# Optimization experiments

Measured on AMD Instinct MI355X. Metric: run time of the kernel, lower is better.

## Reference

```python
import jax, jax.numpy as jnp
import numpy as np

N = 50000      # nodes
E = 800000     # edges (avg degree 16)
NE = 100000    # query edges
IN = 128; HID = 128; OUT = 128; FEAT = 2


def _linear_params(k, fan_in, fan_out):
    # torch.nn.Linear default init: U(-1/sqrt(fan_in), 1/sqrt(fan_in))
    s = 1.0 / np.sqrt(fan_in)
    k1, k2 = jax.random.split(k)
    W = jax.random.uniform(k1, (fan_in, fan_out), jnp.float32, -s, s)
    b = jax.random.uniform(k2, (fan_out,), jnp.float32, -s, s)
    return W, b


def setup_inputs() -> dict:
    key = jax.random.key(0)
    ks = jax.random.split(key, 9)
    inp = {}
    inp["x"] = jax.random.normal(ks[0], (N, IN), jnp.float32)
    inp["adj_t"] = jax.random.randint(ks[1], (2, E), 0, N)          # edge_index [2,E]
    inp["train_edges"] = jax.random.randint(ks[2], (NE, 2), 0, N)   # query edges
    # GCNConv stack params (lin weight + bias per layer)
    inp["W1"], inp["b1"] = _linear_params(ks[3], IN, HID)
    inp["W2"], inp["b2"] = _linear_params(ks[4], HID, HID)
    inp["W3"], inp["b3"] = _linear_params(ks[5], HID, OUT)
    # LinkPredictor MLP params
    inp["P1"], inp["pb1"] = _linear_params(ks[6], OUT, HID)
    inp["P2"], inp["pb2"] = _linear_params(ks[7], HID, HID)
    inp["P3"], inp["pb3"] = _linear_params(ks[8], HID, FEAT)
    return inp


def gcn_conv(x, edge_index, W, b):
    # GCNConv(normalize=False), edge_weight=None:
    #   h = x @ W; out[dst] += h[src]; out += bias
    h = x @ W                                    # [N, d_out]
    msg = h[edge_index[0]]                       # gather  [E, d_out]
    out = jax.ops.segment_sum(msg, edge_index[1], num_segments=x.shape[0])
    return out + b


def reference(x, adj_t, train_edges, W1, b1, W2, b2, W3, b3, P1, pb1, P2, pb2, P3, pb3):
    # GCN trunk (eval mode -> dropout is identity; dropout=0 anyway)
    h = jax.nn.relu(gcn_conv(x, adj_t, W1, b1))
    h = jax.nn.relu(gcn_conv(h, adj_t, W2, b2))
    emb = gcn_conv(h, adj_t, W3, b3)             # [N, OUT]
    # LinkPredictor on (src, dst) node-embedding pairs
    z = emb[train_edges[:, 0]] * emb[train_edges[:, 1]]   # [NE, OUT]
    z = jax.nn.relu(z @ P1 + pb1)
    z = jax.nn.relu(z @ P2 + pb2)
    z = z @ P3 + pb3                                       # [NE, FEAT]
    # F.normalize(p=2, dim=-1) with eps=1e-12
    z = z / jnp.maximum(jnp.linalg.norm(z, axis=-1, keepdims=True), 1e-12)
    pred = jax.nn.log_softmax(z, axis=-1)
    return pred[None]                                      # torch.unsqueeze(pred, 0)
```

## Files before the change

kernel.cpp:

```cpp
#include <hip/hip_runtime.h>
#include <math.h>

#define N_NODES 50000
#define N_EDGES 800000
#define N_QE    100000
#define D       128
#define NB      391
#define PCHUNK  8192

typedef _Float16 half8 __attribute__((ext_vector_type(8)));
typedef short    short8 __attribute__((ext_vector_type(8)));
typedef float    f32x4 __attribute__((ext_vector_type(4)));

static __device__ inline short f2bf(float f) {
    unsigned u = __builtin_bit_cast(unsigned, f);
    u += 0x7FFFu + ((u >> 16) & 1u);
    return (short)(u >> 16);
}

static const size_t O_BCNT = 0;
static const size_t O_OFF  = 256u * 1024;
static const size_t O_BC   = 512u * 1024;
static const size_t O_BB   = 768u * 1024;
static const size_t O_SRC  = 1024u * 1024;
static const size_t O_TMP  = 4u << 20;
static const size_t O_G    = 8u << 20;
static const size_t O_H    = O_G + 12800000u;
static const size_t O_T    = O_H + 12800000u;


__global__ __launch_bounds__(256)
void k_bcount(const int* __restrict__ dst, int* __restrict__ bcnt) {
    __shared__ int h[NB];
    const int t = threadIdx.x;
    const int e0 = blockIdx.x * PCHUNK;
    const int e1 = (e0 + PCHUNK < N_EDGES) ? e0 + PCHUNK : N_EDGES;
    for (int b = t; b < NB; b += 256) h[b] = 0;
    __syncthreads();
    for (int e = e0 + t; e < e1; e += 256)
        atomicAdd(&h[dst[e] >> 7], 1);
    __syncthreads();
    for (int b = t; b < NB; b += 256)
        if (h[b]) atomicAdd(&bcnt[b], h[b]);
}

__global__ __launch_bounds__(512)
void k_bscan(const int* __restrict__ bcnt, int* __restrict__ bbase,
             int* __restrict__ bcur, int* __restrict__ off) {
    __shared__ int sh[512];
    const int t = threadIdx.x;
    int v = (t < NB) ? bcnt[t] : 0;
    sh[t] = v;
    __syncthreads();
    #pragma unroll
    for (int o = 1; o < 512; o <<= 1) {
        int u = (t >= o) ? sh[t - o] : 0;
        __syncthreads();
        sh[t] += u;
        __syncthreads();
    }
    if (t < NB) { int e = sh[t] - v; bbase[t] = e; bcur[t] = e; }
    if (t == 0) { bbase[NB] = N_EDGES; off[N_NODES] = N_EDGES; }
}

__global__ __launch_bounds__(256)
void k_part(const int* __restrict__ src, const int* __restrict__ dst,
            int* __restrict__ bcur, unsigned* __restrict__ tmp)
{
    __shared__ int hcnt[NB];
    __shared__ int lpos[NB];
    __shared__ int base[NB];
    const int t = threadIdx.x;
    const int e0 = blockIdx.x * PCHUNK;
    const int e1 = (e0 + PCHUNK < N_EDGES) ? e0 + PCHUNK : N_EDGES;

    for (int b = t; b < NB; b += 256) { hcnt[b] = 0; lpos[b] = 0; }
    __syncthreads();
    for (int e = e0 + t; e < e1; e += 256)
        atomicAdd(&hcnt[dst[e] >> 7], 1);
    __syncthreads();
    for (int b = t; b < NB; b += 256) {
        int c = hcnt[b];
        base[b] = c ? atomicAdd(&bcur[b], c) : 0;
    }
    __syncthreads();
    for (int e = e0 + t; e < e1; e += 256) {
        int d = dst[e];
        int b = d >> 7;
        int pos = atomicAdd(&lpos[b], 1);
        tmp[base[b] + pos] = (unsigned)src[e] | ((unsigned)(d & 127) << 16);
    }
}

__global__ __launch_bounds__(256)
void k_fine2(const unsigned* __restrict__ tmp, const int* __restrict__ bbase,
             unsigned short* __restrict__ srcs, int* __restrict__ off)
{
    __shared__ int ncnt[128];
    __shared__ int fcur[128];
    const int t = threadIdx.x;
    const int b = blockIdx.x;
    const int n0 = b << 7;
    const int nn = (N_NODES - n0 < 128) ? N_NODES - n0 : 128;
    const int r0 = bbase[b];
    const int r1 = bbase[b + 1];

    if (t < 128) ncnt[t] = 0;
    __syncthreads();
    for (int i = r0 + t; i < r1; i += 256)
        atomicAdd(&ncnt[tmp[i] >> 16], 1);
    __syncthreads();
    int c = (t < 128) ? ncnt[t] : 0;
    #pragma unroll
    for (int o = 1; o < 128; o <<= 1) {
        int u = (t >= o && t < 128) ? ncnt[t - o] : 0;
        __syncthreads();
        if (t < 128) ncnt[t] += u;
        __syncthreads();
    }
    if (t < 128) {
        int excl = r0 + ncnt[t] - c;
        fcur[t] = excl;
        if (t < nn) off[n0 + t] = excl;
    }
    __syncthreads();
    for (int i = r0 + t; i < r1; i += 256) {
        unsigned en = tmp[i];
        int p = atomicAdd(&fcur[en >> 16], 1);
        srcs[p] = (unsigned short)(en & 0xFFFFu);
    }
}

__global__ __launch_bounds__(256)
void k_t16all(const float* __restrict__ W1, const float* __restrict__ W2,
              const float* __restrict__ W3, const float* __restrict__ Q1,
              const float* __restrict__ Q2, short* __restrict__ T)
{
    int m = blockIdx.x >> 6;
    const float* S = (m == 0) ? W1 : (m == 1) ? W2 : (m == 2) ? W3
                   : (m == 3) ? Q1 : Q2;
    short* Dp = T + m * 16384;
    int idx = (blockIdx.x & 63) * 256 + threadIdx.x;
    int c = idx & 127, k = idx >> 7;
    Dp[c * 128 + k] = f2bf(S[k * 128 + c]);
}


template<typename XT>
__global__ __launch_bounds__(256)
void k_mm(const XT* __restrict__ X, const short* __restrict__ WT,
          _Float16* __restrict__ Y, int rows)
{
    __shared__ __align__(16) short xs[64 * 128];
    const int tid = threadIdx.x;
    const int l   = tid & 63;
    const int w   = tid >> 6;
    const int g   = l >> 4;
    const int l15 = l & 15;
    const int row0 = blockIdx.x * 64;

    {
        int r = tid >> 2;
        int gr = row0 + r; if (gr >= rows) gr = rows - 1;
        const XT* src = X + (size_t)gr * D;
        #pragma unroll
        for (int it = 0; it < 4; ++it) {
            int s = (tid & 3) + it * 4;
            short8 h;
            if constexpr (sizeof(XT) == 4) {
                float4 v0 = *(const float4*)((const float*)src + s * 8);
                float4 v1 = *(const float4*)((const float*)src + s * 8 + 4);
                h[0] = f2bf(v0.x); h[1] = f2bf(v0.y);
                h[2] = f2bf(v0.z); h[3] = f2bf(v0.w);
                h[4] = f2bf(v1.x); h[5] = f2bf(v1.y);
                h[6] = f2bf(v1.z); h[7] = f2bf(v1.w);
            } else {
                half8 v = *(const half8*)((const _Float16*)src + s * 8);
                #pragma unroll
                for (int c = 0; c < 8; ++c) h[c] = f2bf((float)v[c]);
            }
            *(short8*)&xs[r * 128 + ((s ^ (r & 7)) * 8)] = h;
        }
    }

    short8 wf[2][4];
    #pragma unroll
    for (int tt = 0; tt < 2; ++tt) {
        int c = w * 32 + tt * 16 + l15;
        #pragma unroll
        for (int s = 0; s < 4; ++s)
            wf[tt][s] = *(const short8*)(WT + (size_t)c * 128 + s * 32 + g * 8);
    }

    __syncthreads();

    f32x4 acc[4][2];
    #pragma unroll
    for (int rt = 0; rt < 4; ++rt)
        #pragma unroll
        for (int tt = 0; tt < 2; ++tt)
            acc[rt][tt] = (f32x4){0.f, 0.f, 0.f, 0.f};

    #pragma unroll
    for (int rt = 0; rt < 4; ++rt) {
        const int r = rt * 16 + l15;
        short8 a[4];
        #pragma unroll
        for (int s = 0; s < 4; ++s) {
            int slot = (4 * s + g) ^ (r & 7);
            a[s] = *(const short8*)&xs[r * 128 + slot * 8];
        }
        #pragma unroll
        for (int tt = 0; tt < 2; ++tt)
            #pragma unroll
            for (int s = 0; s < 4; ++s)
                acc[rt][tt] = __builtin_amdgcn_mfma_f32_16x16x32_bf16(
                    a[s], wf[tt][s], acc[rt][tt], 0, 0, 0);
    }

    __syncthreads();

    #pragma unroll
    for (int rt = 0; rt < 4; ++rt)
        #pragma unroll
        for (int tt = 0; tt < 2; ++tt) {
            int c = w * 32 + tt * 16 + l15;
            #pragma unroll
            for (int i = 0; i < 4; ++i) {
                int row = rt * 16 + g * 4 + i;
                int slot = (c >> 3) ^ (row & 7);
                xs[row * 128 + slot * 8 + (c & 7)] =
                    (short)__builtin_bit_cast(unsigned short, (_Float16)acc[rt][tt][i]);
            }
        }
    __syncthreads();

    {
        int r = tid >> 2;
        int gr = row0 + r;
        if (gr < rows) {
            short* dstp = (short*)(Y + (size_t)gr * D);
            #pragma unroll
            for (int it = 0; it < 4; ++it) {
                int s = (tid & 3) + it * 4;
                *(short8*)(dstp + s * 8) =
                    *(const short8*)&xs[r * 128 + ((s ^ (r & 7)) * 8)];
            }
        }
    }
}

template<bool RELU>
__global__ __launch_bounds__(256)
void k_agg(const _Float16* __restrict__ Hin, const int* __restrict__ off,
           const unsigned short* __restrict__ srcs, const float* __restrict__ bias,
           _Float16* __restrict__ Hout)
{
    const int lane = threadIdx.x & 63;
    const int es   = lane >> 4;
    const int q    = lane & 15;
    const int wv   = threadIdx.x >> 6;
    const int n    = blockIdx.x * 4 + wv;
    const int j0 = __builtin_amdgcn_readfirstlane(off[n]);
    const int j1 = __builtin_amdgcn_readfirstlane(off[n + 1]);

    float acc[8] = {};
    int j = j0;

    for (; j + 16 <= j1; j += 16) {
        half8 v[4];
        #pragma unroll
        for (int k = 0; k < 4; ++k) {
            int s = srcs[j + 4 * k + es];
            v[k] = *(const half8*)(Hin + (size_t)s * D + q * 8);
        }
        #pragma unroll
        for (int k = 0; k < 4; ++k)
            #pragma unroll
            for (int c = 0; c < 8; ++c) acc[c] += (float)v[k][c];
    }
    for (; j + 4 <= j1; j += 4) {
        int s = srcs[j + es];
        half8 v = *(const half8*)(Hin + (size_t)s * D + q * 8);
        #pragma unroll
        for (int c = 0; c < 8; ++c) acc[c] += (float)v[c];
    }
    {
        int rem = j1 - j;
        if (rem > 0) {
            int s = srcs[j + (es < rem ? es : rem - 1)];
            half8 v = *(const half8*)(Hin + (size_t)s * D + q * 8);
            if (es < rem) {
                #pragma unroll
                for (int c = 0; c < 8; ++c) acc[c] += (float)v[c];
            }
        }
    }

    #pragma unroll
    for (int c = 0; c < 8; ++c) {
        acc[c] += __shfl_xor(acc[c], 16, 64);
        acc[c] += __shfl_xor(acc[c], 32, 64);
    }

    if (es == 0) {
        half8 o;
        #pragma unroll
        for (int c = 0; c < 8; ++c) {
            float t = acc[c] + bias[q * 8 + c];
            if (RELU) t = fmaxf(t, 0.f);
            o[c] = (_Float16)t;
        }
        *(half8*)(Hout + (size_t)n * D + q * 8) = o;
    }
}

__global__ __launch_bounds__(256)
void k_predm(const _Float16* __restrict__ emb, const int* __restrict__ te,
             const short* __restrict__ P1T, const float* __restrict__ pb1,
             const short* __restrict__ P2T, const float* __restrict__ pb2,
             const float* __restrict__ P3, const float* __restrict__ pb3,
             float* __restrict__ out)
{
    __shared__ __align__(16) short xs[64 * 128];
    __shared__ float red[64][8];
    const int tid = threadIdx.x;
    const int l   = tid & 63;
    const int w   = tid >> 6;
    const int g   = l >> 4;
    const int l15 = l & 15;
    const int row0 = blockIdx.x * 64;

    {
        int r = tid >> 2;
        int e = row0 + r; if (e >= N_QE) e = N_QE - 1;
        const int2 ee = *(const int2*)(te + 2 * e);
        const _Float16* sp = emb + (size_t)ee.x * D;
        const _Float16* dp = emb + (size_t)ee.y * D;
        #pragma unroll
        for (int it = 0; it < 4; ++it) {
            int s = (tid & 3) + it * 4;
            half8 a = *(const half8*)(sp + s * 8);
            half8 b = *(const half8*)(dp + s * 8);
            short8 h;
            #pragma unroll
            for (int c = 0; c < 8; ++c) h[c] = f2bf((float)a[c] * (float)b[c]);
            *(short8*)&xs[r * 128 + ((s ^ (r & 7)) * 8)] = h;
        }
    }
    __syncthreads();

    f32x4 acc[4][2];

    {
        short8 wf[2][4];
        #pragma unroll
        for (int tt = 0; tt < 2; ++tt) {
            int c = w * 32 + tt * 16 + l15;
            #pragma unroll
            for (int s = 0; s < 4; ++s)
                wf[tt][s] = *(const short8*)(P1T + (size_t)c * 128 + s * 32 + g * 8);
        }
        #pragma unroll
        for (int rt = 0; rt < 4; ++rt)
            #pragma unroll
            for (int tt = 0; tt < 2; ++tt)
                acc[rt][tt] = (f32x4){0.f, 0.f, 0.f, 0.f};

        #pragma unroll
        for (int rt = 0; rt < 4; ++rt) {
            const int r = rt * 16 + l15;
            short8 a[4];
            #pragma unroll
            for (int s = 0; s < 4; ++s) {
                int slot = (4 * s + g) ^ (r & 7);
                a[s] = *(const short8*)&xs[r * 128 + slot * 8];
            }
            #pragma unroll
            for (int tt = 0; tt < 2; ++tt)
                #pragma unroll
                for (int s = 0; s < 4; ++s)
                    acc[rt][tt] = __builtin_amdgcn_mfma_f32_16x16x32_bf16(
                        a[s], wf[tt][s], acc[rt][tt], 0, 0, 0);
        }

        float bv[2];
        #pragma unroll
        for (int tt = 0; tt < 2; ++tt) bv[tt] = pb1[w * 32 + tt * 16 + l15];

        __syncthreads();

        #pragma unroll
        for (int rt = 0; rt < 4; ++rt)
            #pragma unroll
            for (int tt = 0; tt < 2; ++tt) {
                int c = w * 32 + tt * 16 + l15;
                #pragma unroll
                for (int i = 0; i < 4; ++i) {
                    float v = fmaxf(acc[rt][tt][i] + bv[tt], 0.f);
                    int row = rt * 16 + g * 4 + i;
                    int slot = (c >> 3) ^ (row & 7);
                    xs[row * 128 + slot * 8 + (c & 7)] = f2bf(v);
                }
            }
        __syncthreads();
    }

    {
        short8 wf[2][4];
        #pragma unroll
        for (int tt = 0; tt < 2; ++tt) {
            int c = w * 32 + tt * 16 + l15;
            #pragma unroll
            for (int s = 0; s < 4; ++s)
                wf[tt][s] = *(const short8*)(P2T + (size_t)c * 128 + s * 32 + g * 8);
        }
        #pragma unroll
        for (int rt = 0; rt < 4; ++rt)
            #pragma unroll
            for (int tt = 0; tt < 2; ++tt)
                acc[rt][tt] = (f32x4){0.f, 0.f, 0.f, 0.f};

        #pragma unroll
        for (int rt = 0; rt < 4; ++rt) {
            const int r = rt * 16 + l15;
            short8 a[4];
            #pragma unroll
            for (int s = 0; s < 4; ++s) {
                int slot = (4 * s + g) ^ (r & 7);
                a[s] = *(const short8*)&xs[r * 128 + slot * 8];
            }
            #pragma unroll
            for (int tt = 0; tt < 2; ++tt)
                #pragma unroll
                for (int s = 0; s < 4; ++s)
                    acc[rt][tt] = __builtin_amdgcn_mfma_f32_16x16x32_bf16(
                        a[s], wf[tt][s], acc[rt][tt], 0, 0, 0);
        }
    }

    {
        float bv[2];
        float2 p3v[2];
        #pragma unroll
        for (int tt = 0; tt < 2; ++tt) {
            int c = w * 32 + tt * 16 + l15;
            bv[tt] = pb2[c];
            p3v[tt] = *(const float2*)(P3 + c * 2);
        }
        #pragma unroll
        for (int rt = 0; rt < 4; ++rt)
            #pragma unroll
            for (int i = 0; i < 4; ++i) {
                float z0 = fmaxf(acc[rt][0][i] + bv[0], 0.f);
                float z1 = fmaxf(acc[rt][1][i] + bv[1], 0.f);
                float p0 = z0 * p3v[0].x + z1 * p3v[1].x;
                float p1 = z0 * p3v[0].y + z1 * p3v[1].y;
                #pragma unroll
                for (int o = 1; o < 16; o <<= 1) {
                    p0 += __shfl_xor(p0, o, 64);
                    p1 += __shfl_xor(p1, o, 64);
                }
                if (l15 == 0) {
                    int row = rt * 16 + g * 4 + i;
                    red[row][w * 2]     = p0;
                    red[row][w * 2 + 1] = p1;
                }
            }
    }
    __syncthreads();

    if (tid < 64) {
        int gr = row0 + tid;
        if (gr < N_QE) {
            float p0 = red[tid][0] + red[tid][2] + red[tid][4] + red[tid][6] + pb3[0];
            float p1 = red[tid][1] + red[tid][3] + red[tid][5] + red[tid][7] + pb3[1];
            float nrm = fmaxf(sqrtf(p0 * p0 + p1 * p1), 1e-12f);
            p0 /= nrm; p1 /= nrm;
            float m = fmaxf(p0, p1);
            float lse = m + logf(expf(p0 - m) + expf(p1 - m));
            out[gr * 2]     = p0 - lse;
            out[gr * 2 + 1] = p1 - lse;
        }
    }
}

extern "C" void kernel_launch(void* const* d_in, const int* in_sizes, int n_in,
                              void* d_out, int out_size, void* d_ws, size_t ws_size,
                              hipStream_t stream)
{
    (void)in_sizes; (void)n_in; (void)out_size; (void)ws_size;
    const float* x   = (const float*)d_in[0];
    const int*   adj = (const int*)d_in[1];
    const int*   te  = (const int*)d_in[2];
    const float* W1  = (const float*)d_in[3];
    const float* b1  = (const float*)d_in[4];
    const float* W2  = (const float*)d_in[5];
    const float* b2  = (const float*)d_in[6];
    const float* W3  = (const float*)d_in[7];
    const float* b3  = (const float*)d_in[8];
    const float* P1  = (const float*)d_in[9];
    const float* pb1 = (const float*)d_in[10];
    const float* P2  = (const float*)d_in[11];
    const float* pb2 = (const float*)d_in[12];
    const float* P3  = (const float*)d_in[13];
    const float* pb3 = (const float*)d_in[14];
    float* out = (float*)d_out;

    char* ws = (char*)d_ws;
    int* bcnt = (int*)(ws + O_BCNT);
    int* off  = (int*)(ws + O_OFF);
    int* bcur = (int*)(ws + O_BC);
    int* bbase= (int*)(ws + O_BB);
    unsigned short* srcs = (unsigned short*)(ws + O_SRC);
    unsigned* tmp = (unsigned*)(ws + O_TMP);
    _Float16* G = (_Float16*)(ws + O_G);
    _Float16* H = (_Float16*)(ws + O_H);
    short*    T = (short*)(ws + O_T);

    const int* esrc = adj;
    const int* edst = adj + N_EDGES;
    const int NCHUNK = (N_EDGES + PCHUNK - 1) / PCHUNK;

    k_t16all<<<320, 256, 0, stream>>>(W1, W2, W3, P1, P2, T);

    hipMemsetAsync(bcnt, 0, NB * sizeof(int), stream);
    k_bcount<<<NCHUNK, 256, 0, stream>>>(edst, bcnt);
    k_bscan<<<1, 512, 0, stream>>>(bcnt, bbase, bcur, off);
    k_part<<<NCHUNK, 256, 0, stream>>>(esrc, edst, bcur, tmp);
    k_fine2<<<NB, 256, 0, stream>>>(tmp, bbase, srcs, off);

    const int gN = (N_NODES + 63) / 64;

    k_mm<float><<<gN, 256, 0, stream>>>(x, T, H, N_NODES);
    k_agg<true><<<N_NODES / 4, 256, 0, stream>>>(H, off, srcs, b1, G);
    k_mm<_Float16><<<gN, 256, 0, stream>>>(G, T + 16384, H, N_NODES);
    k_agg<true><<<N_NODES / 4, 256, 0, stream>>>(H, off, srcs, b2, G);
    k_mm<_Float16><<<gN, 256, 0, stream>>>(G, T + 2 * 16384, H, N_NODES);
    k_agg<false><<<N_NODES / 4, 256, 0, stream>>>(H, off, srcs, b3, G);

    const int gQ = (N_QE + 63) / 64;
    k_predm<<<gQ, 256, 0, stream>>>(G, te, T + 3 * 16384, pb1,
                                    T + 4 * 16384, pb2, P3, pb3, out);
}
```

Before: 298.6 us.

## Fuse aggregation and linear transform per GCN layer using aggregate-then-multiply order

Each GCN layer now aggregates neighbor features first and then multiplies by W, which is valid because the sum is linear. Aggregation and the MFMA matmul run in one kernel: 64 aggregated rows go straight into shared memory, and bias plus ReLU are applied after the matmul. This removes one launch per layer and the H round-trip to global memory between the matmul and aggregation kernels. In exchange, a small cast kernel now converts x to fp16 first, and each block serialises the aggregation of 8 rows per wave before the MFMA phase, which may reduce the number of gathers in flight.

```diff
diff --git a/kernel.cpp b/kernel.cpp
--- a/kernel.cpp
+++ b/kernel.cpp
@@ -145,11 +145,25 @@
     Dp[c * 128 + k] = f2bf(S[k * 128 + c]);
 }
 
-
-template<typename XT>
 __global__ __launch_bounds__(256)
-void k_mm(const XT* __restrict__ X, const short* __restrict__ WT,
-          _Float16* __restrict__ Y, int rows)
+void k_cast(const float* __restrict__ X, _Float16* __restrict__ Y) {
+    int i = (blockIdx.x * 256 + threadIdx.x) * 8;
+    float4 v0 = *(const float4*)(X + i);
+    float4 v1 = *(const float4*)(X + i + 4);
+    half8 h;
+    h[0] = (_Float16)v0.x; h[1] = (_Float16)v0.y;
+    h[2] = (_Float16)v0.z; h[3] = (_Float16)v0.w;
+    h[4] = (_Float16)v1.x; h[5] = (_Float16)v1.y;
+    h[6] = (_Float16)v1.z; h[7] = (_Float16)v1.w;
+    *(half8*)(Y + i) = h;
+}
+
+
+template<bool RELU>
+__global__ __launch_bounds__(512)
+void k_fagg(const _Float16* __restrict__ Xin, const int* __restrict__ off,
+            const unsigned short* __restrict__ srcs, const short* __restrict__ WT,
+            const float* __restrict__ bias, _Float16* __restrict__ Y, int rows)
 {
     __shared__ __align__(16) short xs[64 * 128];
     const int tid = threadIdx.x;
@@ -159,48 +173,67 @@
     const int l15 = l & 15;
     const int row0 = blockIdx.x * 64;
 
-    {
-        int r = tid >> 2;
-        int gr = row0 + r; if (gr >= rows) gr = rows - 1;
-        const XT* src = X + (size_t)gr * D;
-        #pragma unroll
-        for (int it = 0; it < 4; ++it) {
-            int s = (tid & 3) + it * 4;
+    short8 wf[4];
+    {
+        int c = w * 16 + l15;
+        #pragma unroll
+        for (int s = 0; s < 4; ++s)
+            wf[s] = *(const short8*)(WT + (size_t)c * 128 + s * 32 + g * 8);
+    }
+
+    for (int i = 0; i < 8; ++i) {
+        const int r = w * 8 + i;
+        const int n = row0 + r;
+        float acc[8] = {};
+        if (n < rows) {
+            const int j0 = __builtin_amdgcn_readfirstlane(off[n]);
+            const int j1 = __builtin_amdgcn_readfirstlane(off[n + 1]);
+            int j = j0;
+            for (; j + 16 <= j1; j += 16) {
+                half8 v[4];
+                #pragma unroll
+                for (int k = 0; k < 4; ++k) {
+                    int s = srcs[j + 4 * k + g];
+                    v[k] = *(const half8*)(Xin + (size_t)s * D + l15 * 8);
+                }
+                #pragma unroll
+                for (int k = 0; k < 4; ++k)
+                    #pragma unroll
+                    for (int c = 0; c < 8; ++c) acc[c] += (float)v[k][c];
+            }
+            for (; j + 4 <= j1; j += 4) {
+                int s = srcs[j + g];
+                half8 v = *(const half8*)(Xin + (size_t)s * D + l15 * 8);
+                #pragma unroll
+                for (int c = 0; c < 8; ++c) acc[c] += (float)v[c];
+            }
+            int rem = j1 - j;
+            if (rem > 0) {
+                int s = srcs[j + (g < rem ? g : rem - 1)];
+                half8 v = *(const half8*)(Xin + (size_t)s * D + l15 * 8);
+                if (g < rem) {
+                    #pragma unroll
+                    for (int c = 0; c < 8; ++c) acc[c] += (float)v[c];
+                }
+            }
+        }
+        #pragma unroll
+        for (int c = 0; c < 8; ++c) {
+            acc[c] += __shfl_xor(acc[c], 16, 64);
+            acc[c] += __shfl_xor(acc[c], 32, 64);
+        }
+        if (g == 0) {
             short8 h;
-            if constexpr (sizeof(XT) == 4) {
-                float4 v0 = *(const float4*)((const float*)src + s * 8);
-                float4 v1 = *(const float4*)((const float*)src + s * 8 + 4);
-                h[0] = f2bf(v0.x); h[1] = f2bf(v0.y);
-                h[2] = f2bf(v0.z); h[3] = f2bf(v0.w);
-                h[4] = f2bf(v1.x); h[5] = f2bf(v1.y);
-                h[6] = f2bf(v1.z); h[7] = f2bf(v1.w);
-            } else {
-                half8 v = *(const half8*)((const _Float16*)src + s * 8);
-                #pragma unroll
-                for (int c = 0; c < 8; ++c) h[c] = f2bf((float)v[c]);
-            }
-            *(short8*)&xs[r * 128 + ((s ^ (r & 7)) * 8)] = h;
-        }
-    }
-
-    short8 wf[2][4];
+            #pragma unroll
+            for (int c = 0; c < 8; ++c) h[c] = f2bf(acc[c]);
+            *(short8*)&xs[r * 128 + ((l15 ^ (r & 7)) * 8)] = h;
+        }
+    }
+    __syncthreads();
+
+    f32x4 acc2[4];
     #pragma unroll
-    for (int tt = 0; tt < 2; ++tt) {
-        int c = w * 32 + tt * 16 + l15;
-        #pragma unroll
-        for (int s = 0; s < 4; ++s)
-            wf[tt][s] = *(const short8*)(WT + (size_t)c * 128 + s * 32 + g * 8);
-    }
-
-    __syncthreads();
-
-    f32x4 acc[4][2];
-    #pragma unroll
-    for (int rt = 0; rt < 4; ++rt)
-        #pragma unroll
-        for (int tt = 0; tt < 2; ++tt)
-            acc[rt][tt] = (f32x4){0.f, 0.f, 0.f, 0.f};
-
+    for (int rt = 0; rt < 4; ++rt) acc2[rt] = (f32x4){0.f, 0.f, 0.f, 0.f};
     #pragma unroll
     for (int rt = 0; rt < 4; ++rt) {
         const int r = rt * 16 + l15;
@@ -211,107 +244,41 @@
             a[s] = *(const short8*)&xs[r * 128 + slot * 8];
         }
         #pragma unroll
-        for (int tt = 0; tt < 2; ++tt)
-            #pragma unroll
-            for (int s = 0; s < 4; ++s)
-                acc[rt][tt] = __builtin_amdgcn_mfma_f32_16x16x32_bf16(
-                    a[s], wf[tt][s], acc[rt][tt], 0, 0, 0);
-    }
-
-    __syncthreads();
-
-    #pragma unroll
-    for (int rt = 0; rt < 4; ++rt)
-        #pragma unroll
-        for (int tt = 0; tt < 2; ++tt) {
-            int c = w * 32 + tt * 16 + l15;
+        for (int s = 0; s < 4; ++s)
+            acc2[rt] = __builtin_amdgcn_mfma_f32_16x16x32_bf16(
+                a[s], wf[s], acc2[rt], 0, 0, 0);
+    }
+    __syncthreads();
+
+    {
+        const int c = w * 16 + l15;
+        const float bv = bias[c];
+        #pragma unroll
+        for (int rt = 0; rt < 4; ++rt)
             #pragma unroll
             for (int i = 0; i < 4; ++i) {
+                float v = acc2[rt][i] + bv;
+                if (RELU) v = fmaxf(v, 0.f);
                 int row = rt * 16 + g * 4 + i;
                 int slot = (c >> 3) ^ (row & 7);
                 xs[row * 128 + slot * 8 + (c & 7)] =
-                    (short)__builtin_bit_cast(unsigned short, (_Float16)acc[rt][tt][i]);
-            }
-        }
-    __syncthreads();
-
-    {
-        int r = tid >> 2;
+                    (short)__builtin_bit_cast(unsigned short, (_Float16)v);
+            }
+    }
+    __syncthreads();
+
+    {
+        int r = tid >> 3;
         int gr = row0 + r;
         if (gr < rows) {
             short* dstp = (short*)(Y + (size_t)gr * D);
             #pragma unroll
-            for (int it = 0; it < 4; ++it) {
-                int s = (tid & 3) + it * 4;
+            for (int it = 0; it < 2; ++it) {
+                int s = (tid & 7) + it * 8;
                 *(short8*)(dstp + s * 8) =
                     *(const short8*)&xs[r * 128 + ((s ^ (r & 7)) * 8)];
             }
         }
-    }
-}
-
-template<bool RELU>
-__global__ __launch_bounds__(256)
-void k_agg(const _Float16* __restrict__ Hin, const int* __restrict__ off,
-           const unsigned short* __restrict__ srcs, const float* __restrict__ bias,
-           _Float16* __restrict__ Hout)
-{
-    const int lane = threadIdx.x & 63;
-    const int es   = lane >> 4;
-    const int q    = lane & 15;
-    const int wv   = threadIdx.x >> 6;
-    const int n    = blockIdx.x * 4 + wv;
-    const int j0 = __builtin_amdgcn_readfirstlane(off[n]);
-    const int j1 = __builtin_amdgcn_readfirstlane(off[n + 1]);
-
-    float acc[8] = {};
-    int j = j0;
-
-    for (; j + 16 <= j1; j += 16) {
-        half8 v[4];
-        #pragma unroll
-        for (int k = 0; k < 4; ++k) {
-            int s = srcs[j + 4 * k + es];
-            v[k] = *(const half8*)(Hin + (size_t)s * D + q * 8);
-        }
-        #pragma unroll
-        for (int k = 0; k < 4; ++k)
-            #pragma unroll
-            for (int c = 0; c < 8; ++c) acc[c] += (float)v[k][c];
-    }
-    for (; j + 4 <= j1; j += 4) {
-        int s = srcs[j + es];
-        half8 v = *(const half8*)(Hin + (size_t)s * D + q * 8);
-        #pragma unroll
-        for (int c = 0; c < 8; ++c) acc[c] += (float)v[c];
-    }
-    {
-        int rem = j1 - j;
-        if (rem > 0) {
-            int s = srcs[j + (es < rem ? es : rem - 1)];
-            half8 v = *(const half8*)(Hin + (size_t)s * D + q * 8);
-            if (es < rem) {
-                #pragma unroll
-                for (int c = 0; c < 8; ++c) acc[c] += (float)v[c];
-            }
-        }
-    }
-
-    #pragma unroll
-    for (int c = 0; c < 8; ++c) {
-        acc[c] += __shfl_xor(acc[c], 16, 64);
-        acc[c] += __shfl_xor(acc[c], 32, 64);
-    }
-
-    if (es == 0) {
-        half8 o;
-        #pragma unroll
-        for (int c = 0; c < 8; ++c) {
-            float t = acc[c] + bias[q * 8 + c];
-            if (RELU) t = fmaxf(t, 0.f);
-            o[c] = (_Float16)t;
-        }
-        *(half8*)(Hout + (size_t)n * D + q * 8) = o;
     }
 }
 
@@ -530,16 +497,15 @@
     k_part<<<NCHUNK, 256, 0, stream>>>(esrc, edst, bcur, tmp);
     k_fine2<<<NB, 256, 0, stream>>>(tmp, bbase, srcs, off);
 
+    k_cast<<<(N_NODES * D) / (256 * 8), 256, 0, stream>>>(x, G);
+
     const int gN = (N_NODES + 63) / 64;
 
-    k_mm<float><<<gN, 256, 0, stream>>>(x, T, H, N_NODES);
-    k_agg<true><<<N_NODES / 4, 256, 0, stream>>>(H, off, srcs, b1, G);
-    k_mm<_Float16><<<gN, 256, 0, stream>>>(G, T + 16384, H, N_NODES);
-    k_agg<true><<<N_NODES / 4, 256, 0, stream>>>(H, off, srcs, b2, G);
-    k_mm<_Float16><<<gN, 256, 0, stream>>>(G, T + 2 * 16384, H, N_NODES);
-    k_agg<false><<<N_NODES / 4, 256, 0, stream>>>(H, off, srcs, b3, G);
+    k_fagg<true ><<<gN, 512, 0, stream>>>(G, off, srcs, T,             b1, H, N_NODES);
+    k_fagg<true ><<<gN, 512, 0, stream>>>(H, off, srcs, T + 16384,     b2, G, N_NODES);
+    k_fagg<false><<<gN, 512, 0, stream>>>(G, off, srcs, T + 2 * 16384, b3, H, N_NODES);
 
     const int gQ = (N_QE + 63) / 64;
-    k_predm<<<gQ, 256, 0, stream>>>(G, te, T + 3 * 16384, pb1,
+    k_predm<<<gQ, 256, 0, stream>>>(H, te, T + 3 * 16384, pb1,
                                     T + 4 * 16384, pb2, P3, pb3, out);
 }
```

After: 333.4 us. +11.6%, slower.
